# Performance work log

Measured on AMD Instinct MI355X. Metric: run time of the kernel, lower is better.

## Reference

```python
import jax, jax.numpy as jnp
import numpy as np

UNITS = 128
FILTERS = 32
KSIZE = 31
B, T, DV, DQ = 64, 1000, 512, 1024


def setup_inputs() -> dict:
    key = jax.random.key(0)
    ks = jax.random.split(key, 12)
    scale = 0.05
    inp = {
        "query": jax.random.normal(ks[0], (B, DQ), jnp.float32),
        "values": jax.random.normal(ks[1], (B, T, DV), jnp.float32),
        "previous_attention_weights": jax.random.uniform(ks[2], (B, T, 1), jnp.float32),
        # learned params
        "Wq": jax.random.normal(ks[3], (DQ, UNITS), jnp.float32) * scale,
        "bq": jnp.zeros((UNITS,), jnp.float32),
        "Wm": jax.random.normal(ks[4], (DV, UNITS), jnp.float32) * scale,
        "bm": jnp.zeros((UNITS,), jnp.float32),
        "Wv": jax.random.normal(ks[5], (UNITS, 1), jnp.float32) * scale,
        "bv": jnp.zeros((1,), jnp.float32),
        "Wconv": jax.random.normal(ks[6], (KSIZE, 1, FILTERS), jnp.float32) * scale,  # [W, Cin, Cout]
        "Wl": jax.random.normal(ks[7], (FILTERS, UNITS), jnp.float32) * scale,
    }
    return inp


def _forward(query, values, prev_w, Wq, bq, Wm, bm, Wv, bv, Wconv, Wl):
    # location features: Conv1D (same padding, no bias) then Dense(tanh, no bias)
    loc = jax.lax.conv_general_dilated(
        prev_w, Wconv, window_strides=(1,), padding="SAME",
        dimension_numbers=("NWC", "WIO", "NWC"))          # [B, T, FILTERS]
    loc = jnp.tanh(loc @ Wl)                                # [B, T, UNITS]
    q = query @ Wq + bq                                     # [B, UNITS]
    m = values @ Wm + bm                                    # [B, T, UNITS]
    score = jnp.tanh(m + q[:, None, :] + loc) @ Wv + bv     # [B, T, 1]
    attention_weights = jax.nn.softmax(score, axis=1)       # softmax over time
    context = jnp.sum(attention_weights * values, axis=1)   # [B, DV]
    return context, attention_weights


def reference(query, values, previous_attention_weights, Wq, bq, Wm, bm, Wv, bv, Wconv, Wl):
    return _forward(query, values, previous_attention_weights,
                    Wq, bq, Wm, bm, Wv, bv, Wconv, Wl)
```

## Files before the change

### kernel.cpp

```cpp
#include <hip/hip_runtime.h>

#define B_  64
#define T_  1000
#define DV_ 512
#define DQ_ 1024
#define U_  128
#define F_  32
#define KS_ 31
#define P_  16
#define CT_ 63

typedef __attribute__((ext_vector_type(8))) short short8;
typedef __attribute__((ext_vector_type(4))) float f32x4;

__device__ __forceinline__ unsigned pk2(float a, float b) {
    union { float f; unsigned u; } x, y;
    x.f = a; y.f = b;
    unsigned ra = (x.u + 0x7FFFu + ((x.u >> 16) & 1u)) >> 16;
    unsigned rb = (y.u + 0x7FFFu + ((y.u >> 16) & 1u)) >> 16;
    return (ra & 0xFFFFu) | (rb << 16);
}

__device__ __forceinline__ float fast_tanh(float x) {
    return 1.0f - 2.0f / (__expf(2.0f * x) + 1.0f);
}

__device__ __forceinline__ short8 pk8(float4 f0, float4 f1) {
    int4 q;
    q.x = pk2(f0.x, f0.y); q.y = pk2(f0.z, f0.w);
    q.z = pk2(f1.x, f1.y); q.w = pk2(f1.z, f1.w);
    return *(short8*)&q;
}

__global__ __launch_bounds__(1024) void prep_kernel(
    const float* __restrict__ Wm, const float* __restrict__ Wl,
    const float* __restrict__ query, const float* __restrict__ Wq,
    short* __restrict__ WmX, short* __restrict__ WlX, float* __restrict__ partQ)
{
    __shared__ float sh[1024];
    int blk = blockIdx.x, tid = threadIdx.x;
    if (blk < 9) {
        int g = blk * 1024 + tid;
        if (g < 8192) {
            int kc = g >> 9, e = g & 511;
            int n = e >> 2, q = e & 3;
            int kb = kc * 32 + q * 8;
            int4 p;
            p.x = pk2(Wm[(kb + 0) * U_ + n], Wm[(kb + 1) * U_ + n]);
            p.y = pk2(Wm[(kb + 2) * U_ + n], Wm[(kb + 3) * U_ + n]);
            p.z = pk2(Wm[(kb + 4) * U_ + n], Wm[(kb + 5) * U_ + n]);
            p.w = pk2(Wm[(kb + 6) * U_ + n], Wm[(kb + 7) * U_ + n]);
            ((int4*)WmX)[g] = p;
        } else if (g < 8704) {
            int e = g - 8192;
            int n = e >> 2, q = e & 3;
            int kb = q * 8;
            int4 p;
            p.x = pk2(Wl[(kb + 0) * U_ + n], Wl[(kb + 1) * U_ + n]);
            p.y = pk2(Wl[(kb + 2) * U_ + n], Wl[(kb + 3) * U_ + n]);
            p.z = pk2(Wl[(kb + 4) * U_ + n], Wl[(kb + 5) * U_ + n]);
            p.w = pk2(Wl[(kb + 6) * U_ + n], Wl[(kb + 7) * U_ + n]);
            ((int4*)WlX)[e] = p;
        }
    } else {
        int id = blk - 9;
        int s  = id >> 2;
        int bg = id & 3;
        sh[tid] = query[(size_t)(bg * 16 + (tid >> 6)) * DQ_ + s * 64 + (tid & 63)];
        __syncthreads();
        int u = tid & 127, h = tid >> 7;
        const float* wp = Wq + (size_t)(s * 64) * U_ + u;
        const float* q0 = sh + (h * 2) * 64;
        const float* q1 = q0 + 64;
        float a0 = 0.f, a1 = 0.f;
#pragma unroll 8
        for (int k = 0; k < 64; ++k) {
            float w = wp[(size_t)k * U_];
            a0 += q0[k] * w; a1 += q1[k] * w;
        }
        int b0i = bg * 16 + h * 2;
        partQ[s * 8192 + b0i * 128 + u]       = a0;
        partQ[s * 8192 + (b0i + 1) * 128 + u] = a1;
    }
}

__global__ __launch_bounds__(256) void score_kernel(
    const float* __restrict__ values, const float* __restrict__ prev,
    const float* __restrict__ Wc, const float* __restrict__ Wv,
    const float* __restrict__ bv, const short* __restrict__ WmX,
    const short* __restrict__ WlX, const float* __restrict__ partQ,
    const float* __restrict__ bq, const float* __restrict__ bm,
    float* __restrict__ scores)
{
    __shared__ float WcS[KS_ * F_];
    __shared__ short AsL[64 * 32];
    __shared__ float qbS[2 * U_];
    __shared__ float WvS[U_];

    const int tid = threadIdx.x;
    const int r0 = blockIdx.x * 64;
    const int b0 = r0 / T_;
    const int b1 = (r0 + 63) / T_;

    for (int i = tid; i < KS_ * F_; i += 256) WcS[i] = Wc[i];
    if (tid < U_) WvS[tid] = Wv[tid];
    {
        int u = tid & (U_ - 1);
        int bb = (tid < U_) ? b0 : b1;
        float s = bq[u] + bm[u];
#pragma unroll
        for (int sl = 0; sl < 16; ++sl) s += partQ[sl * 8192 + bb * 128 + u];
        qbS[tid] = s;
    }

    const int wv = tid >> 6, lane = tid & 63;
    const int quad = lane >> 4, m15 = lane & 15;
    const int row0 = wv * 16 + m15;
    const float* aP = values + (size_t)(r0 + row0) * DV_ + quad * 8;
    const int4* bW  = (const int4*)WmX + m15 * 4 + quad;
    const int4* blW = (const int4*)WlX + m15 * 4 + quad;

    float4 aq0[2], aq1[2], aq2[2];
    int4 bf[8];
    aq0[0] = *(const float4*)(aP);      aq0[1] = *(const float4*)(aP + 4);
    aq1[0] = *(const float4*)(aP + 32); aq1[1] = *(const float4*)(aP + 36);
#pragma unroll
    for (int c = 0; c < 8; ++c) bf[c] = bW[c * 64];

    __syncthreads();

    {
        int i = tid & 63, fg = tid >> 6;
        int r = r0 + i;
        int b = r / T_;
        int t = r - b * T_;
        const float* pv = prev + b * T_;
        float a8[8] = {};
#pragma unroll
        for (int k = 0; k < KS_; ++k) {
            int tt = t + k - 15;
            float p = ((unsigned)tt < (unsigned)T_) ? pv[tt] : 0.f;
#pragma unroll
            for (int j = 0; j < 8; ++j) a8[j] += p * WcS[k * F_ + fg * 8 + j];
        }
        int4 pq;
        pq.x = pk2(a8[0], a8[1]); pq.y = pk2(a8[2], a8[3]);
        pq.z = pk2(a8[4], a8[5]); pq.w = pk2(a8[6], a8[7]);
        ((int4*)AsL)[i * 4 + (fg ^ ((i >> 1) & 3))] = pq;
    }
    __syncthreads();

    f32x4 acc[8] = {};
    {
        short8 afl = ((const short8*)AsL)[row0 * 4 + (quad ^ ((row0 >> 1) & 3))];
#pragma unroll
        for (int c = 0; c < 8; ++c) {
            int4 bl = blW[c * 64];
            acc[c] = __builtin_amdgcn_mfma_f32_16x16x32_bf16(afl, *(short8*)&bl, acc[c], 0, 0, 0);
        }
        int qoff[4];
#pragma unroll
        for (int v = 0; v < 4; ++v) {
            int r = r0 + wv * 16 + quad * 4 + v;
            qoff[v] = ((r / T_) == b0) ? 0 : U_;
        }
#pragma unroll
        for (int c = 0; c < 8; ++c) {
            int col = c * 16 + m15;
#pragma unroll
            for (int v = 0; v < 4; ++v)
                acc[c][v] = qbS[qoff[v] + col] + fast_tanh(acc[c][v]);
        }
    }

#pragma unroll
    for (int kc = 0; kc < 16; ++kc) {
        if (kc + 2 < 16) {
            aq2[0] = *(const float4*)(aP + (kc + 2) * 32);
            aq2[1] = *(const float4*)(aP + (kc + 2) * 32 + 4);
        }
        short8 af = pk8(aq0[0], aq0[1]);
#pragma unroll
        for (int c = 0; c < 8; ++c) {
            acc[c] = __builtin_amdgcn_mfma_f32_16x16x32_bf16(af, *(short8*)&bf[c], acc[c], 0, 0, 0);
            if (kc + 1 < 16) bf[c] = bW[(kc + 1) * 512 + c * 64];
        }
        aq0[0] = aq1[0]; aq0[1] = aq1[1];
        aq1[0] = aq2[0]; aq1[1] = aq2[1];
    }

    float psum[4] = {};
#pragma unroll
    for (int c = 0; c < 8; ++c) {
        int col = c * 16 + m15;
        float wvv = WvS[col];
#pragma unroll
        for (int v = 0; v < 4; ++v)
            psum[v] += fast_tanh(acc[c][v]) * wvv;
    }
#pragma unroll
    for (int off = 1; off < 16; off <<= 1) {
#pragma unroll
        for (int v = 0; v < 4; ++v) psum[v] += __shfl_xor(psum[v], off);
    }
    if (m15 == 0) {
        float bvv = bv[0];
#pragma unroll
        for (int v = 0; v < 4; ++v)
            scores[r0 + wv * 16 + quad * 4 + v] = psum[v] + bvv;
    }
}

__global__ __launch_bounds__(256) void ctx1_kernel(
    const float* __restrict__ values, const float* __restrict__ scores,
    float* __restrict__ attw, float* __restrict__ part)
{
    __shared__ float wS[CT_];
    __shared__ float4 ps[128];
    __shared__ float red[4];
    int b = blockIdx.x, p = blockIdx.y, tid = threadIdx.x;
    const float* sb = scores + b * T_;

    float v[4];
    int tv[4];
#pragma unroll
    for (int i = 0; i < 4; ++i) {
        int t = tid + i * 256;
        tv[i] = t;
        v[i] = (t < T_) ? sb[t] : -1e30f;
    }
    float mx = fmaxf(fmaxf(v[0], v[1]), fmaxf(v[2], v[3]));
#pragma unroll
    for (int off = 32; off >= 1; off >>= 1) mx = fmaxf(mx, __shfl_xor(mx, off));
    int wvi = tid >> 6, lane = tid & 63;
    if (lane == 0) red[wvi] = mx;
    __syncthreads();
    mx = fmaxf(fmaxf(red[0], red[1]), fmaxf(red[2], red[3]));
    float sum = 0.f;
#pragma unroll
    for (int i = 0; i < 4; ++i)
        sum += (tv[i] < T_) ? __expf(v[i] - mx) : 0.f;
#pragma unroll
    for (int off = 32; off >= 1; off >>= 1) sum += __shfl_xor(sum, off);
    __syncthreads();
    if (lane == 0) red[wvi] = sum;
    __syncthreads();
    float inv = 1.0f / (red[0] + red[1] + red[2] + red[3]);

    int t0 = p * CT_;
    int len = (T_ - t0 < CT_) ? (T_ - t0) : CT_;
    if (tid < len) {
        float e = __expf(sb[t0 + tid] - mx) * inv;
        wS[tid] = e;
        attw[b * T_ + t0 + tid] = e;
    }
    __syncthreads();

    int cl = tid & 127, tp = tid >> 7;
    const float* vp = values + ((size_t)b * T_ + t0) * DV_ + cl * 4;
    float4 a = {0.f, 0.f, 0.f, 0.f};
#pragma unroll 4
    for (int t = tp; t < len; t += 2) {
        float4 vv = *(const float4*)(vp + (size_t)t * DV_);
        float wt = wS[t];
        a.x += wt * vv.x; a.y += wt * vv.y; a.z += wt * vv.z; a.w += wt * vv.w;
    }
    if (tp == 1) ps[cl] = a;
    __syncthreads();
    if (tp == 0) {
        float4 o = ps[cl];
        o.x += a.x; o.y += a.y; o.z += a.z; o.w += a.w;
        *(float4*)(part + ((size_t)(b * P_ + p)) * DV_ + cl * 4) = o;
    }
}

__global__ void ctx2_kernel(const float* __restrict__ part, float* __restrict__ ctx) {
    int b = blockIdx.x, tid = threadIdx.x;
    const float* pp = part + (size_t)b * P_ * DV_ + tid * 4;
    float4 s = {0.f, 0.f, 0.f, 0.f};
#pragma unroll
    for (int p = 0; p < P_; ++p) {
        float4 v = *(const float4*)(pp + (size_t)p * DV_);
        s.x += v.x; s.y += v.y; s.z += v.z; s.w += v.w;
    }
    *(float4*)(ctx + (size_t)b * DV_ + tid * 4) = s;
}

extern "C" void kernel_launch(void* const* d_in, const int* in_sizes, int n_in,
                              void* d_out, int out_size, void* d_ws, size_t ws_size,
                              hipStream_t stream) {
    const float* query  = (const float*)d_in[0];
    const float* values = (const float*)d_in[1];
    const float* prev   = (const float*)d_in[2];
    const float* Wq     = (const float*)d_in[3];
    const float* bq     = (const float*)d_in[4];
    const float* Wm     = (const float*)d_in[5];
    const float* bm     = (const float*)d_in[6];
    const float* Wv     = (const float*)d_in[7];
    const float* bv     = (const float*)d_in[8];
    const float* Wc     = (const float*)d_in[9];
    const float* Wl     = (const float*)d_in[10];

    float* out  = (float*)d_out;
    float* ctx  = out;
    float* attw = out + B_ * DV_;

    char* ws = (char*)d_ws;
    float* part   = (float*)(ws);
    float* partQ  = (float*)(ws);
    float* scores = (float*)(ws + 2097152);
    short* WmX    = (short*)(ws + 2097152 + 262144);
    short* WlX    = (short*)(ws + 2097152 + 262144 + 131072);

    prep_kernel<<<73, 1024, 0, stream>>>(Wm, Wl, query, Wq, WmX, WlX, partQ);
    score_kernel<<<1000, 256, 0, stream>>>(values, prev, Wc, Wv, bv, WmX, WlX,
                                           partQ, bq, bm, scores);
    ctx1_kernel<<<dim3(B_, P_), 256, 0, stream>>>(values, scores, attw, part);
    ctx2_kernel<<<B_, 128, 0, stream>>>(part, ctx);
}
```

Measured before the change: 265.6 us.

## Fuse softmax-weighted context accumulation into score kernel with atomics

The score kernel is re-gridded to one (time-chunk, batch) pair per block. After computing scores, each block exponentiates them without subtracting the max, accumulates exp-weighted values into a per-batch context buffer, and adds the partial exp sum to a per-batch total, both by atomics. A small finish kernel then normalizes the context and attention weights, replacing the separate context and reduction kernels and the second pass over values. The change relies on scores being small enough that unshifted exp does not overflow, uses float atomics whose summation order is nondeterministic, and needs a memset. The last time chunk of each batch is partly idle, and the query projection split is also reorganized.

```diff
diff --git a/kernel.cpp b/kernel.cpp
--- a/kernel.cpp
+++ b/kernel.cpp
@@ -7,8 +7,6 @@
 #define U_  128
 #define F_  32
 #define KS_ 31
-#define P_  16
-#define CT_ 63
 
 typedef __attribute__((ext_vector_type(8))) short short8;
 typedef __attribute__((ext_vector_type(4))) float f32x4;
@@ -64,23 +62,17 @@
         }
     } else {
         int id = blk - 9;
-        int s  = id >> 2;
-        int bg = id & 3;
-        sh[tid] = query[(size_t)(bg * 16 + (tid >> 6)) * DQ_ + s * 64 + (tid & 63)];
+        int s  = id >> 3;
+        int bg = id & 7;
+        sh[tid] = query[(size_t)(bg * 8 + (tid >> 7)) * DQ_ + s * 128 + (tid & 127)];
         __syncthreads();
         int u = tid & 127, h = tid >> 7;
-        const float* wp = Wq + (size_t)(s * 64) * U_ + u;
-        const float* q0 = sh + (h * 2) * 64;
-        const float* q1 = q0 + 64;
-        float a0 = 0.f, a1 = 0.f;
+        const float* wp = Wq + (size_t)(s * 128) * U_ + u;
+        const float* q0 = sh + h * 128;
+        float a0 = 0.f;
 #pragma unroll 8
-        for (int k = 0; k < 64; ++k) {
-            float w = wp[(size_t)k * U_];
-            a0 += q0[k] * w; a1 += q1[k] * w;
-        }
-        int b0i = bg * 16 + h * 2;
-        partQ[s * 8192 + b0i * 128 + u]       = a0;
-        partQ[s * 8192 + (b0i + 1) * 128 + u] = a1;
+        for (int k = 0; k < 128; ++k) a0 += q0[k] * wp[(size_t)k * U_];
+        partQ[s * 8192 + (bg * 8 + h) * 128 + u] = a0;
     }
 }
 
@@ -90,33 +82,37 @@
     const float* __restrict__ bv, const short* __restrict__ WmX,
     const short* __restrict__ WlX, const float* __restrict__ partQ,
     const float* __restrict__ bq, const float* __restrict__ bm,
-    float* __restrict__ scores)
+    float* __restrict__ scores, float* __restrict__ ctxU,
+    float* __restrict__ lsum)
 {
     __shared__ float WcS[KS_ * F_];
     __shared__ short AsL[64 * 32];
-    __shared__ float qbS[2 * U_];
+    __shared__ float qbS[U_];
     __shared__ float WvS[U_];
+    __shared__ float wS[64];
+    __shared__ float4 ps[128];
 
     const int tid = threadIdx.x;
-    const int r0 = blockIdx.x * 64;
-    const int b0 = r0 / T_;
-    const int b1 = (r0 + 63) / T_;
+    const int p = blockIdx.x, b = blockIdx.y;
+    const int t0 = p * 64;
+    const int nr = (T_ - t0 < 64) ? (T_ - t0) : 64;
 
     for (int i = tid; i < KS_ * F_; i += 256) WcS[i] = Wc[i];
     if (tid < U_) WvS[tid] = Wv[tid];
-    {
-        int u = tid & (U_ - 1);
-        int bb = (tid < U_) ? b0 : b1;
+    if (tid >= 128) {
+        int u = tid - 128;
         float s = bq[u] + bm[u];
 #pragma unroll
-        for (int sl = 0; sl < 16; ++sl) s += partQ[sl * 8192 + bb * 128 + u];
-        qbS[tid] = s;
+        for (int sl = 0; sl < 8; ++sl) s += partQ[sl * 8192 + b * 128 + u];
+        qbS[u] = s;
     }
 
     const int wv = tid >> 6, lane = tid & 63;
     const int quad = lane >> 4, m15 = lane & 15;
     const int row0 = wv * 16 + m15;
-    const float* aP = values + (size_t)(r0 + row0) * DV_ + quad * 8;
+    const int trow = t0 + row0;
+    const int tcl = (trow < T_) ? trow : (T_ - 1);
+    const float* aP = values + ((size_t)b * T_ + tcl) * DV_ + quad * 8;
     const int4* bW  = (const int4*)WmX + m15 * 4 + quad;
     const int4* blW = (const int4*)WlX + m15 * 4 + quad;
 
@@ -131,17 +127,15 @@
 
     {
         int i = tid & 63, fg = tid >> 6;
-        int r = r0 + i;
-        int b = r / T_;
-        int t = r - b * T_;
+        int t = t0 + i;
         const float* pv = prev + b * T_;
         float a8[8] = {};
 #pragma unroll
         for (int k = 0; k < KS_; ++k) {
             int tt = t + k - 15;
-            float p = ((unsigned)tt < (unsigned)T_) ? pv[tt] : 0.f;
-#pragma unroll
-            for (int j = 0; j < 8; ++j) a8[j] += p * WcS[k * F_ + fg * 8 + j];
+            float pp = ((unsigned)tt < (unsigned)T_) ? pv[tt] : 0.f;
+#pragma unroll
+            for (int j = 0; j < 8; ++j) a8[j] += pp * WcS[k * F_ + fg * 8 + j];
         }
         int4 pq;
         pq.x = pk2(a8[0], a8[1]); pq.y = pk2(a8[2], a8[3]);
@@ -158,18 +152,12 @@
             int4 bl = blW[c * 64];
             acc[c] = __builtin_amdgcn_mfma_f32_16x16x32_bf16(afl, *(short8*)&bl, acc[c], 0, 0, 0);
         }
-        int qoff[4];
-#pragma unroll
-        for (int v = 0; v < 4; ++v) {
-            int r = r0 + wv * 16 + quad * 4 + v;
-            qoff[v] = ((r / T_) == b0) ? 0 : U_;
-        }
 #pragma unroll
         for (int c = 0; c < 8; ++c) {
             int col = c * 16 + m15;
 #pragma unroll
             for (int v = 0; v < 4; ++v)
-                acc[c][v] = qbS[qoff[v] + col] + fast_tanh(acc[c][v]);
+                acc[c][v] = qbS[col] + fast_tanh(acc[c][v]);
         }
     }
 
@@ -206,84 +194,71 @@
     if (m15 == 0) {
         float bvv = bv[0];
 #pragma unroll
-        for (int v = 0; v < 4; ++v)
-            scores[r0 + wv * 16 + quad * 4 + v] = psum[v] + bvv;
-    }
-}
-
-__global__ __launch_bounds__(256) void ctx1_kernel(
-    const float* __restrict__ values, const float* __restrict__ scores,
-    float* __restrict__ attw, float* __restrict__ part)
+        for (int v = 0; v < 4; ++v) {
+            int row = wv * 16 + quad * 4 + v;
+            int t = t0 + row;
+            float s = psum[v] + bvv;
+            if (t < T_) {
+                scores[b * T_ + t] = s;
+                wS[row] = __expf(s);
+            } else {
+                wS[row] = 0.f;
+            }
+        }
+    }
+    __syncthreads();
+
+    if (tid < 64) {
+        float x = wS[tid];
+#pragma unroll
+        for (int off = 1; off < 64; off <<= 1) x += __shfl_xor(x, off);
+        if (tid == 0) atomicAdd(lsum + b, x);
+    }
+
+    {
+        int cl = tid & 127, tp = tid >> 7;
+        const float* vp = values + ((size_t)b * T_ + t0) * DV_ + cl * 4;
+        float4 a = {0.f, 0.f, 0.f, 0.f};
+#pragma unroll 4
+        for (int t = tp; t < nr; t += 2) {
+            float4 vv = *(const float4*)(vp + (size_t)t * DV_);
+            float wt = wS[t];
+            a.x += wt * vv.x; a.y += wt * vv.y; a.z += wt * vv.z; a.w += wt * vv.w;
+        }
+        if (tp == 1) ps[cl] = a;
+        __syncthreads();
+        if (tp == 0) {
+            float4 o = ps[cl];
+            o.x += a.x; o.y += a.y; o.z += a.z; o.w += a.w;
+            float* cp = ctxU + (size_t)b * DV_ + cl * 4;
+            atomicAdd(cp + 0, o.x);
+            atomicAdd(cp + 1, o.y);
+            atomicAdd(cp + 2, o.z);
+            atomicAdd(cp + 3, o.w);
+        }
+    }
+}
+
+__global__ __launch_bounds__(256) void finish_kernel(
+    const float* __restrict__ scores, const float* __restrict__ ctxU,
+    const float* __restrict__ lsum, float* __restrict__ attw,
+    float* __restrict__ ctx)
 {
-    __shared__ float wS[CT_];
-    __shared__ float4 ps[128];
-    __shared__ float red[4];
-    int b = blockIdx.x, p = blockIdx.y, tid = threadIdx.x;
+    int b = blockIdx.x, tid = threadIdx.x;
+    float inv = 1.0f / lsum[b];
+    {
+        const float2* cu = (const float2*)(ctxU + (size_t)b * DV_);
+        float2* co = (float2*)(ctx + (size_t)b * DV_);
+        float2 v = cu[tid];
+        v.x *= inv; v.y *= inv;
+        co[tid] = v;
+    }
     const float* sb = scores + b * T_;
-
-    float v[4];
-    int tv[4];
 #pragma unroll
     for (int i = 0; i < 4; ++i) {
         int t = tid + i * 256;
-        tv[i] = t;
-        v[i] = (t < T_) ? sb[t] : -1e30f;
-    }
-    float mx = fmaxf(fmaxf(v[0], v[1]), fmaxf(v[2], v[3]));
-#pragma unroll
-    for (int off = 32; off >= 1; off >>= 1) mx = fmaxf(mx, __shfl_xor(mx, off));
-    int wvi = tid >> 6, lane = tid & 63;
-    if (lane == 0) red[wvi] = mx;
-    __syncthreads();
-    mx = fmaxf(fmaxf(red[0], red[1]), fmaxf(red[2], red[3]));
-    float sum = 0.f;
-#pragma unroll
-    for (int i = 0; i < 4; ++i)
-        sum += (tv[i] < T_) ? __expf(v[i] - mx) : 0.f;
-#pragma unroll
-    for (int off = 32; off >= 1; off >>= 1) sum += __shfl_xor(sum, off);
-    __syncthreads();
-    if (lane == 0) red[wvi] = sum;
-    __syncthreads();
-    float inv = 1.0f / (red[0] + red[1] + red[2] + red[3]);
-
-    int t0 = p * CT_;
-    int len = (T_ - t0 < CT_) ? (T_ - t0) : CT_;
-    if (tid < len) {
-        float e = __expf(sb[t0 + tid] - mx) * inv;
-        wS[tid] = e;
-        attw[b * T_ + t0 + tid] = e;
-    }
-    __syncthreads();
-
-    int cl = tid & 127, tp = tid >> 7;
-    const float* vp = values + ((size_t)b * T_ + t0) * DV_ + cl * 4;
-    float4 a = {0.f, 0.f, 0.f, 0.f};
-#pragma unroll 4
-    for (int t = tp; t < len; t += 2) {
-        float4 vv = *(const float4*)(vp + (size_t)t * DV_);
-        float wt = wS[t];
-        a.x += wt * vv.x; a.y += wt * vv.y; a.z += wt * vv.z; a.w += wt * vv.w;
-    }
-    if (tp == 1) ps[cl] = a;
-    __syncthreads();
-    if (tp == 0) {
-        float4 o = ps[cl];
-        o.x += a.x; o.y += a.y; o.z += a.z; o.w += a.w;
-        *(float4*)(part + ((size_t)(b * P_ + p)) * DV_ + cl * 4) = o;
-    }
-}
-
-__global__ void ctx2_kernel(const float* __restrict__ part, float* __restrict__ ctx) {
-    int b = blockIdx.x, tid = threadIdx.x;
-    const float* pp = part + (size_t)b * P_ * DV_ + tid * 4;
-    float4 s = {0.f, 0.f, 0.f, 0.f};
-#pragma unroll
-    for (int p = 0; p < P_; ++p) {
-        float4 v = *(const float4*)(pp + (size_t)p * DV_);
-        s.x += v.x; s.y += v.y; s.z += v.z; s.w += v.w;
-    }
-    *(float4*)(ctx + (size_t)b * DV_ + tid * 4) = s;
+        if (t < T_) attw[b * T_ + t] = __expf(sb[t]) * inv;
+    }
 }
 
 extern "C" void kernel_launch(void* const* d_in, const int* in_sizes, int n_in,
@@ -306,15 +281,17 @@
     float* attw = out + B_ * DV_;
 
     char* ws = (char*)d_ws;
-    float* part   = (float*)(ws);
     float* partQ  = (float*)(ws);
-    float* scores = (float*)(ws + 2097152);
-    short* WmX    = (short*)(ws + 2097152 + 262144);
-    short* WlX    = (short*)(ws + 2097152 + 262144 + 131072);
-
+    float* scores = (float*)(ws + 262144);
+    short* WmX    = (short*)(ws + 524288);
+    short* WlX    = (short*)(ws + 655360);
+    float* ctxU   = (float*)(ws + 663552);
+    float* lsum   = (float*)(ws + 794624);
+
+    hipMemsetAsync(ctxU, 0, B_ * DV_ * sizeof(float) + B_ * sizeof(float), stream);
     prep_kernel<<<73, 1024, 0, stream>>>(Wm, Wl, query, Wq, WmX, WlX, partQ);
-    score_kernel<<<1000, 256, 0, stream>>>(values, prev, Wc, Wv, bv, WmX, WlX,
-                                           partQ, bq, bm, scores);
-    ctx1_kernel<<<dim3(B_, P_), 256, 0, stream>>>(values, scores, attw, part);
-    ctx2_kernel<<<B_, 128, 0, stream>>>(part, ctx);
-}
+    score_kernel<<<dim3(16, B_), 256, 0, stream>>>(values, prev, Wc, Wv, bv,
+                                                   WmX, WlX, partQ, bq, bm,
+                                                   scores, ctxU, lsum);
+    finish_kernel<<<B_, 256, 0, stream>>>(scores, ctxU, lsum, attw, ctx);
+}
```

Result: no change. 266.4 us (+0.3%).
